# Optimization experiments

Measured on AMD Instinct MI355X. Metric: run time of the kernel, lower is better.

The kernel has to match this reference:

```python
import jax, jax.numpy as jnp
import numpy as np

B, N, D, DFC, EMB, L = 16, 1024, 128, 128, 64, 4
NHOPS = (1, 2, 3, 4)  # tatic='cont': nhop(i) = i + 1
EDGE_P = 0.03


def _make_adj(k):
    u = jax.random.uniform(k, (B, N, N))
    a = u < EDGE_P
    a = a | jnp.transpose(a, (0, 2, 1))          # undirected
    a = a | jnp.eye(N, dtype=bool)[None]         # self loops
    return a.astype(jnp.float32)


def setup_inputs() -> dict:
    key = jax.random.key(0)
    ks = jax.random.split(key, 16)
    s = 0.05
    x = jax.random.normal(ks[0], (B, N, 2 * EMB), jnp.float32)
    adj1 = _make_adj(ks[1])
    adj2 = _make_adj(ks[2])
    valid = jnp.ones((B, N), jnp.float32)
    embede_w = jax.random.normal(ks[3], (D, 2 * EMB)) * s
    gW = jax.random.normal(ks[4], (L, D, D)) * s
    gb = jnp.zeros((L, D), jnp.float32)
    gA = jax.random.normal(ks[5], (L, D, D)) * s
    gate_w = jax.random.normal(ks[6], (L, 1, 2 * D)) * s
    gate_b = jnp.zeros((L, 1), jnp.float32)
    fc0_w = jax.random.normal(ks[7], (DFC, D)) * s
    fc0_b = jnp.zeros((DFC,), jnp.float32)
    fc1_w = jax.random.normal(ks[8], (DFC, DFC)) * s
    fc1_b = jnp.zeros((DFC,), jnp.float32)
    fc2_w = jax.random.normal(ks[9], (DFC, DFC)) * s
    fc2_b = jnp.zeros((DFC,), jnp.float32)
    fc3_w = jax.random.normal(ks[10], (1, DFC)) * s
    fc3_b = jnp.zeros((1,), jnp.float32)
    return dict(x=x, adj1=adj1, adj2=adj2, valid=valid, embede_w=embede_w,
                gW=gW, gb=gb, gA=gA, gate_w=gate_w, gate_b=gate_b,
                fc0_w=fc0_w, fc0_b=fc0_b, fc1_w=fc1_w, fc1_b=fc1_b,
                fc2_w=fc2_w, fc2_b=fc2_b, fc3_w=fc3_w, fc3_b=fc3_b)


def _glema(x, adj, W, b, A, gw, gbias, nhop):
    h = x @ W.T + b                                        # [B,N,D]
    e = jnp.einsum('bjl,bkl->bjk', jnp.einsum('bjd,de->bje', h, A), h)
    e = e + jnp.transpose(e, (0, 2, 1))                    # undirected
    att = jnp.where(adj > 0, e, jnp.float32(0.0))
    att = jax.nn.softmax(att, axis=1) * adj                # softmax over dim 1, then adj mask
    az = jax.nn.relu(jnp.einsum('bij,bjd->bid', att, h))
    coeff = jax.nn.sigmoid(jnp.concatenate([h, az], -1) @ gw.T + gbias)  # [B,N,1]
    z = h
    for _ in range(nhop):
        az = jax.nn.relu(jnp.einsum('bij,bjd->bid', att, z))
        z = coeff * h + (1.0 - coeff) * az
    return z


def reference(x, adj1, adj2, valid, embede_w, gW, gb, gA, gate_w, gate_b,
              fc0_w, fc0_b, fc1_w, fc1_b, fc2_w, fc2_b, fc3_w, fc3_b):
    h = x @ embede_w.T                                     # embede (no bias)
    for k in range(L):                                     # branch='both': c_hs2 - c_hs1
        h1 = _glema(h, adj1, gW[k], gb[k], gA[k], gate_w[k], gate_b[k], NHOPS[k])
        h2 = _glema(h, adj2, gW[k], gb[k], gA[k], gate_w[k], gate_b[k], NHOPS[k])
        h = h2 - h1                                        # dropout p used in eval mode -> identity
    h = h * valid[..., None]
    pooled = h.sum(1) / valid.sum(1, keepdims=True)        # [B,D]
    y = jax.nn.relu(pooled @ fc0_w.T + fc0_b)
    y = jax.nn.relu(y @ fc1_w.T + fc1_b)
    y = jax.nn.relu(y @ fc2_w.T + fc2_b)
    y = jax.nn.sigmoid(y @ fc3_w.T + fc3_b)
    return y.reshape(-1)                                   # [B]
```

## Files before the change

### kernel.cpp

```cpp
#include <hip/hip_runtime.h>

typedef _Float16 half_t;
typedef _Float16 half8 __attribute__((ext_vector_type(8)));
typedef _Float16 half4v __attribute__((ext_vector_type(4)));
typedef float floatx4 __attribute__((ext_vector_type(4)));

#define MFMA(a,b,c) __builtin_amdgcn_mfma_f32_16x16x32_f16(a,b,c,0,0,0)

#define NB 16
#define NLEN 1024
#define DD 128
#define BN (NB*NLEN)
#define BND ((size_t)NB*NLEN*DD)
#define BNN ((size_t)NB*NLEN*NLEN)
#define ELLS 128
#define EMP 1044

static __device__ inline half_t f16h(unsigned pk) {
    unsigned short us = (unsigned short)(pk & 0xffffu);
    half_t h; __builtin_memcpy(&h, &us, 2); return h;
}

__global__ __launch_bounds__(256)
void k_pre(const float* __restrict__ adj1, const float* __restrict__ adj2,
           unsigned* __restrict__ ell, unsigned* __restrict__ cntA,
           const float* __restrict__ x, const float* __restrict__ Ew, half_t* __restrict__ h16,
           const float* __restrict__ gW, const float* __restrict__ gA,
           half_t* __restrict__ Wf, half_t* __restrict__ STf) {
    int tid = threadIdx.x;
    int bid = blockIdx.x;
    if (bid < 8192) {
        __shared__ unsigned ebuf[4][ELLS];
        int w = tid >> 6, l = tid & 63;
        int R = bid * 4 + w;
        int br = R >> 14, nb = R & 16383;
        const float* arow = (br ? adj2 : adj1) + (size_t)nb * 1024;
        unsigned* myb = ebuf[w];
        myb[l] = 0u; myb[l + 64] = 0u;
        float4 v0 = *(const float4*)&arow[l * 4];
        float4 v1 = *(const float4*)&arow[256 + l * 4];
        float4 v2 = *(const float4*)&arow[512 + l * 4];
        float4 v3 = *(const float4*)&arow[768 + l * 4];
        unsigned long long lmask = (l == 0) ? 0ull : (~0ull >> (64 - l));
        int base = 0;
        float vals[16] = {v0.x, v0.y, v0.z, v0.w, v1.x, v1.y, v1.z, v1.w,
                          v2.x, v2.y, v2.z, v2.w, v3.x, v3.y, v3.z, v3.w};
#pragma unroll
        for (int ch = 0; ch < 4; ch++) {
#pragma unroll
            for (int comp = 0; comp < 4; comp++) {
                bool pred = vals[ch * 4 + comp] > 0.f;
                unsigned long long b = __ballot(pred);
                if (pred) {
                    int idx = base + __popcll(b & lmask);
                    if (idx < ELLS) myb[idx] = ((unsigned)(ch * 256 + l * 4 + comp)) << 16;
                }
                base += __popcll(b);
            }
        }
        if (base > ELLS) base = ELLS;
        if (l == 0) cntA[R] = (unsigned)base;
        uint2 o = {myb[l * 2], myb[l * 2 + 1]};
        *(uint2*)&ell[(size_t)R * ELLS + l * 2] = o;
        return;
    }
    if (bid >= 10240) {
        int i = (bid - 10240) * 256 + tid;
        Wf[i] = (half_t)gW[i];
        int base = i & ~16383;
        int lrem = i & 16383;
        int d = lrem >> 7, e = lrem & 127;
        STf[base + (e << 7) + d] = (half_t)(gA[i] + gA[base + (e << 7) + d]);
        return;
    }
    __shared__ float rows[8][DD];
    int g = (bid - 8192) * 8;
    {
        int nl = tid >> 5, c4 = (tid & 31) * 4;
        *(float4*)&rows[nl][c4] = *(const float4*)&x[(size_t)(g + nl) * DD + c4];
    }
    __syncthreads();
    int t = tid & 127, half = tid >> 7;
    const float* wr = Ew + (size_t)t * DD;
    float acc[4] = {0.f, 0.f, 0.f, 0.f};
    for (int k = 0; k < DD; k++) {
        float w = wr[k];
#pragma unroll
        for (int m = 0; m < 4; m++) acc[m] += rows[half + 2 * m][k] * w;
    }
#pragma unroll
    for (int m = 0; m < 4; m++) h16[(size_t)(g + half + 2 * m) * DD + t] = (half_t)acc[m];
}

__global__ __launch_bounds__(256)
void k_proj(const half_t* __restrict__ pa, const half_t* __restrict__ pb,
            const half_t* __restrict__ Wf, const float* __restrict__ bias,
            const half_t* __restrict__ STf,
            half_t* __restrict__ hbr16, half_t* __restrict__ hbrF, half_t* __restrict__ hSF) {
    __shared__ half_t htile[32 * 136];
    __shared__ half_t hbtile[32 * 136];
    int g = blockIdx.x * 32;
    int t = threadIdx.x;
    int w = t >> 6, l = t & 63, q = l >> 4, l15 = l & 15;
#pragma unroll
    for (int v = 0; v < 2; v++) {
        int idx = v * 256 + t; int r = idx >> 4, c8 = (idx & 15) * 8;
        half8 va = *(const half8*)&pa[((size_t)(g + r) << 7) + c8];
        if (pb) {
            half8 vb = *(const half8*)&pb[((size_t)(g + r) << 7) + c8];
            va = va - vb;
        }
        *(half8*)&htile[r * 136 + c8] = va;
    }
    __syncthreads();
    int rowh = (w & 1) * 16;
    int c0 = (w >> 1) * 4;
    half8 a1[4];
#pragma unroll
    for (int kc = 0; kc < 4; kc++) a1[kc] = *(const half8*)&htile[(rowh + l15) * 136 + kc * 32 + q * 8];
    floatx4 acc[4];
#pragma unroll
    for (int cc = 0; cc < 4; cc++) {
        int col = (c0 + cc) * 16 + l15;
        floatx4 a = {0.f, 0.f, 0.f, 0.f};
#pragma unroll
        for (int kc = 0; kc < 4; kc++) {
            half8 bf = *(const half8*)&Wf[((size_t)col << 7) + kc * 32 + q * 8];
            a = MFMA(a1[kc], bf, a);
        }
        float bv = bias[col];
        a.x += bv; a.y += bv; a.z += bv; a.w += bv;
        acc[cc] = a;
    }
#pragma unroll
    for (int cc = 0; cc < 4; cc++) {
        int col = (c0 + cc) * 16 + l15;
#pragma unroll
        for (int r = 0; r < 4; r++)
            hbtile[(rowh + q * 4 + r) * 136 + col] = (half_t)acc[cc][r];
    }
    __syncthreads();
    half8 a2[4];
#pragma unroll
    for (int kc = 0; kc < 4; kc++) a2[kc] = *(const half8*)&hbtile[(rowh + l15) * 136 + kc * 32 + q * 8];
#pragma unroll
    for (int cc = 0; cc < 4; cc++) {
        int col = (c0 + cc) * 16 + l15;
        floatx4 a = {0.f, 0.f, 0.f, 0.f};
#pragma unroll
        for (int kc = 0; kc < 4; kc++) {
            half8 bf = *(const half8*)&STf[((size_t)col << 7) + kc * 32 + q * 8];
            a = MFMA(a2[kc], bf, a);
        }
        acc[cc] = a;
    }
    __syncthreads();
#pragma unroll
    for (int cc = 0; cc < 4; cc++) {
        int col = (c0 + cc) * 16 + l15;
#pragma unroll
        for (int r = 0; r < 4; r++) htile[(rowh + q * 4 + r) * 136 + col] = (half_t)acc[cc][r];
    }
    __syncthreads();
#pragma unroll
    for (int v = 0; v < 2; v++) {
        int idx = v * 256 + t; int r = idx >> 4, c8 = (idx & 15) * 8;
        *(half8*)&hbr16[((size_t)(g + r) << 7) + c8] = *(const half8*)&hbtile[r * 136 + c8];
    }
#pragma unroll
    for (int v = 0; v < 2; v++) {
        int fi = v * 256 + t;
        int g2 = fi >> 8, kc = (fi >> 6) & 3, li = fi & 63;
        int src = (g2 * 16 + (li & 15)) * 136 + kc * 32 + (li >> 4) * 8;
        size_t dst = (((size_t)(blockIdx.x * 2 + g2) * 4 + kc) << 10) + li * 8;
        *(half8*)&hbrF[dst] = *(const half8*)&hbtile[src];
        *(half8*)&hSF[dst]  = *(const half8*)&htile[src];
    }
}

__global__ __launch_bounds__(256)
void k_E(const half_t* __restrict__ hSF, const half_t* __restrict__ hbrF,
         const half_t* __restrict__ hbr16,
         unsigned* __restrict__ ell, const unsigned* __restrict__ cntA,
         float* __restrict__ rsr, half_t* __restrict__ hbrs) {
    int b = blockIdx.y, s = blockIdx.x;
    int t = threadIdx.x, w = t >> 6, l = t & 63, q = l >> 4, l15 = l & 15;
    __shared__ half_t emS[16 * EMP];
    __shared__ float rsS[2][16];
    size_t Gb = (size_t)b * 64;
    half8 A[4];
#pragma unroll
    for (int kc = 0; kc < 4; kc++)
        A[kc] = *(const half8*)&hSF[(((Gb + s) * 4 + kc) << 10) + l * 8];
#pragma unroll 4
    for (int cg = 0; cg < 16; cg++) {
        int c0 = w * 256 + cg * 16;
        floatx4 a = {0.f, 0.f, 0.f, 0.f};
#pragma unroll
        for (int kc = 0; kc < 4; kc++) {
            half8 bf = *(const half8*)&hbrF[(((Gb + w * 16 + cg) * 4 + kc) << 10) + l * 8];
            a = MFMA(A[kc], bf, a);
        }
#pragma unroll
        for (int r = 0; r < 4; r++)
            emS[(q * 4 + r) * EMP + c0 + l15] = (half_t)a[r];
    }
    __syncthreads();
    const float CN = 0.000335462627903f;
#pragma unroll
    for (int rr = 0; rr < 4; rr++) {
        int rl = w * 4 + rr;
        int rowg = b * 1024 + s * 16 + rl;
#pragma unroll
        for (int br = 0; br < 2; br++) {
            size_t R = ((size_t)br << 14) + rowg;
            int cn = (int)cntA[R];
            float rs = 0.f;
            for (int base = 0; base < cn; base += 64) {
                int si = base + l;
                float v = 0.f;
                if (si < cn) {
                    unsigned pk = ell[R * ELLS + si];
                    int col = (int)(pk >> 16);
                    float em = (float)emS[rl * EMP + col];
                    v = __expf(em - 8.f);
                    half_t hv = (half_t)v;
                    unsigned short us; __builtin_memcpy(&us, &hv, 2);
                    ((unsigned short*)ell)[(R * ELLS + si) * 2] = us;
                }
                rs += v;
            }
            rs += __shfl_xor(rs, 1); rs += __shfl_xor(rs, 2);
            rs += __shfl_xor(rs, 4); rs += __shfl_xor(rs, 8);
            rs += __shfl_xor(rs, 16); rs += __shfl_xor(rs, 32);
            if (l == 0) {
                float rv = 1.f / (rs + (1024.f - (float)cn) * CN);
                rsr[R] = rv;
                rsS[br][rl] = rv;
            }
        }
    }
    __syncthreads();
    const half_t* hrow = hbr16 + ((size_t)b << 17) + ((size_t)(s * 16) << 7);
#pragma unroll
    for (int v = 0; v < 2; v++) {
        int idx = v * 256 + t;
        int row = idx >> 5, br2 = (idx >> 4) & 1, ch = idx & 15;
        half8 hv = *(const half8*)&hrow[(size_t)row * 128 + ch * 8];
        float sc = rsS[br2][row];
        half8 o;
#pragma unroll
        for (int d = 0; d < 8; d++) o[d] = (half_t)(sc * (float)hv[d]);
        *(half8*)&hbrs[(size_t)br2 * BND + ((size_t)(b * 1024 + s * 16 + row) << 7) + ch * 8] = o;
    }
}

__global__ __launch_bounds__(256)
void k_az(const unsigned* __restrict__ ell, const unsigned* __restrict__ cntA,
          const float* __restrict__ rsr,
          const half_t* __restrict__ zin, const half_t* __restrict__ hbr16,
          const float* __restrict__ gw, const float* __restrict__ gb_,
          float* __restrict__ cfb, half_t* __restrict__ outp, int mode) {
    int t = threadIdx.x, w = t >> 6, l = t & 63;
    int g = l >> 4, l15 = l & 15;
    int R = blockIdx.x * 16 + w * 4 + g;
    int br = R >> 14, nb = R & 16383;
    const unsigned* ep = ell + (size_t)R * ELLS;
    int cn = (int)cntA[R];
    const half_t* zb = zin + (size_t)br * BND + (((size_t)(nb & ~1023)) << 7) + l15 * 8;
    half8 acc8 = {};
    uint4 p4 = *(const uint4*)ep;
    for (int s = 0; s < cn; s += 4) {
        uint4 cur = p4;
        p4 = *(const uint4*)(ep + s + 4);
        unsigned pk[4] = {cur.x, cur.y, cur.z, cur.w};
#pragma unroll
        for (int i = 0; i < 4; i++) {
            half8 zz = *(const half8*)(zb + (((size_t)(pk[i] >> 16)) << 7));
            half_t hv = f16h(pk[i]);
            half8 vv = {hv, hv, hv, hv, hv, hv, hv, hv};
            acc8 += zz * vv;
        }
    }
    float acc[8];
#pragma unroll
    for (int d = 0; d < 8; d++) acc[d] = fmaxf((float)acc8[d], 0.f);
    half8 hv8 = *(const half8*)&hbr16[((size_t)nb << 7) + l15 * 8];
    float hv[8];
#pragma unroll
    for (int d = 0; d < 8; d++) hv[d] = (float)hv8[d];
    float cf;
    if (mode >= 3) {
        const float* g1 = gw + l15 * 8;
        const float* g2 = gw + 128 + l15 * 8;
        float dp = 0.f;
#pragma unroll
        for (int d = 0; d < 8; d++) dp += hv[d] * g1[d] + acc[d] * g2[d];
        dp += __shfl_xor(dp, 1); dp += __shfl_xor(dp, 2);
        dp += __shfl_xor(dp, 4); dp += __shfl_xor(dp, 8);
        cf = 1.f / (1.f + __expf(-(dp + gb_[0])));
        if (l15 == 0) cfb[R] = cf;
    } else {
        cf = cfb[R];
    }
    float sc = (mode == 1 || mode == 3) ? rsr[R] : 1.f;
    half8 o;
#pragma unroll
    for (int d = 0; d < 8; d++)
        o[d] = (half_t)(sc * (cf * hv[d] + (1.f - cf) * acc[d]));
    *(half8*)&outp[(size_t)R * DD + l15 * 8] = o;
}

__global__ __launch_bounds__(256)
void k_pool(const half_t* __restrict__ z2, const half_t* __restrict__ z1,
            const float* __restrict__ valid, float* __restrict__ part) {
    int b = blockIdx.y, s = blockIdx.x;
    int t = threadIdx.x, d = t & 127, hf = t >> 7;
    __shared__ float red[128];
    float acc = 0.f;
    int nbase = s * 128 + hf * 64;
    for (int n = nbase; n < nbase + 64; n++) {
        size_t gi = ((size_t)(b * 1024 + n) << 7) + d;
        acc += ((float)z2[gi] - (float)z1[gi]) * valid[b * 1024 + n];
    }
    if (hf) red[d] = acc;
    __syncthreads();
    if (!hf) part[(b * 8 + s) * 128 + d] = acc + red[d];
}

__global__ __launch_bounds__(128)
void k_mlp(const float* __restrict__ part, const float* __restrict__ valid,
           const float* __restrict__ w0, const float* __restrict__ b0,
           const float* __restrict__ w1, const float* __restrict__ b1,
           const float* __restrict__ w2, const float* __restrict__ b2,
           const float* __restrict__ w3, const float* __restrict__ b3,
           float* __restrict__ out) {
    int b = blockIdx.x, t = threadIdx.x;
    __shared__ float y0[DD], y1[DD];
    __shared__ float sred[2];
    float vs = 0.f;
    for (int n = t; n < NLEN; n += 128) vs += valid[b * NLEN + n];
    for (int off = 32; off; off >>= 1) vs += __shfl_down(vs, off);
    if ((t & 63) == 0) sred[t >> 6] = vs;
    __syncthreads();
    float vsum = sred[0] + sred[1];
    float acc = 0.f;
#pragma unroll
    for (int s = 0; s < 8; s++) acc += part[(b * 8 + s) * 128 + t];
    y0[t] = acc / vsum;
    __syncthreads();
    float a = b0[t];
    for (int k = 0; k < DD; k++) a += y0[k] * w0[t * DD + k];
    y1[t] = fmaxf(a, 0.f);
    __syncthreads();
    a = b1[t];
    for (int k = 0; k < DD; k++) a += y1[k] * w1[t * DD + k];
    y0[t] = fmaxf(a, 0.f);
    __syncthreads();
    a = b2[t];
    for (int k = 0; k < DD; k++) a += y0[k] * w2[t * DD + k];
    y1[t] = fmaxf(a, 0.f);
    __syncthreads();
    float p = y1[t] * w3[t];
    for (int off = 32; off; off >>= 1) p += __shfl_down(p, off);
    if ((t & 63) == 0) sred[t >> 6] = p;
    __syncthreads();
    if (t == 0) out[b] = 1.f / (1.f + __expf(-(sred[0] + sred[1] + b3[0])));
}

extern "C" void kernel_launch(void* const* d_in, const int* in_sizes, int n_in,
                              void* d_out, int out_size, void* d_ws, size_t ws_size,
                              hipStream_t stream) {
    (void)in_sizes; (void)n_in; (void)out_size; (void)ws_size;
    const float* x     = (const float*)d_in[0];
    const float* adj1  = (const float*)d_in[1];
    const float* adj2  = (const float*)d_in[2];
    const float* valid = (const float*)d_in[3];
    const float* Ew    = (const float*)d_in[4];
    const float* gW    = (const float*)d_in[5];
    const float* gb    = (const float*)d_in[6];
    const float* gA    = (const float*)d_in[7];
    const float* gatew = (const float*)d_in[8];
    const float* gateb = (const float*)d_in[9];
    const float* w0 = (const float*)d_in[10]; const float* b0 = (const float*)d_in[11];
    const float* w1 = (const float*)d_in[12]; const float* b1 = (const float*)d_in[13];
    const float* w2 = (const float*)d_in[14]; const float* b2 = (const float*)d_in[15];
    const float* w3 = (const float*)d_in[16]; const float* b3 = (const float*)d_in[17];
    float* out = (float*)d_out;

    char* p = (char*)d_ws;
    float* rsr  = (float*)p; p += 2 * BN * 4;
    float* cfb  = (float*)p; p += 2 * BN * 4;
    float* partb = (float*)p; p += (size_t)NB * 8 * 128 * 4;
    half_t* h16   = (half_t*)p; p += BND * 2;
    half_t* hbr16 = (half_t*)p; p += BND * 2;
    half_t* hbrF  = (half_t*)p; p += BND * 2;
    half_t* hSF   = (half_t*)p; p += BND * 2;
    half_t* hbrs  = (half_t*)p; p += 2 * BND * 2;
    half_t* zf    = (half_t*)p; p += 2 * BND * 2;
    half_t* zsA   = (half_t*)p; p += 2 * BND * 2;
    half_t* zsB   = (half_t*)p; p += 2 * BND * 2;
    unsigned* ell = (unsigned*)p; p += (size_t)2 * BN * ELLS * 4 + 16;
    unsigned* cntA = (unsigned*)p; p += (size_t)2 * BN * 4;
    half_t* Wf16 = (half_t*)p; p += (size_t)4 * 128 * 128 * 2;
    half_t* ST16 = (half_t*)p; p += (size_t)4 * 128 * 128 * 2;

    k_pre<<<10496, 256, 0, stream>>>(adj1, adj2, ell, cntA, x, Ew, h16, gW, gA, Wf16, ST16);

    for (int k = 0; k < 4; k++) {
        int nhop = k + 1;
        const half_t* pa = k ? (zf + BND) : h16;
        const half_t* pb = k ? zf : nullptr;
        k_proj<<<512, 256, 0, stream>>>(pa, pb, Wf16 + (size_t)k * 16384, gb + k * 128,
                                        ST16 + (size_t)k * 16384, hbr16, hbrF, hSF);
        k_E<<<dim3(64, NB), 256, 0, stream>>>(hSF, hbrF, hbr16, ell, cntA, rsr, hbrs);
        half_t* tgate = (nhop == 1) ? zf : zsA;
        k_az<<<2048, 256, 0, stream>>>(ell, cntA, rsr, hbrs, hbr16,
                                       gatew + k * 256, gateb + k, cfb, tgate,
                                       (nhop == 1) ? 4 : 3);
        half_t* src = tgate;
        for (int hop = 2; hop <= nhop; hop++) {
            half_t* dst = (hop == nhop) ? zf : ((hop & 1) ? zsA : zsB);
            k_az<<<2048, 256, 0, stream>>>(ell, cntA, rsr, src, hbr16,
                                           gatew + k * 256, gateb + k, cfb, dst,
                                           (hop == nhop) ? 2 : 1);
            src = dst;
        }
    }
    k_pool<<<dim3(8, NB), 256, 0, stream>>>(zf + BND, zf, valid, partb);
    k_mlp<<<16, 128, 0, stream>>>(partb, valid, w0, b0, w1, b1, w2, b2, w3, b3, out);
}
```

Measured before the change: 697.4 us.

## Fuse all stages into one persistent cooperative kernel with grid syncs

Replaces the chain of roughly two dozen kernel launches (preprocess, per-layer projection, attention/E, hop aggregation, pooling, MLP) with a single cooperative kernel. Each stage becomes a grid-stride loop over its former blocks, separated by grid-wide barriers, and all stages share one shared-memory union. The aim is to remove launch gaps and the idle tail between dependent kernels. In exchange, the whole kernel must fit the largest stage's shared memory and register footprint, which can lower occupancy for the light aggregation stages, and each grid barrier has its own cost. The original multi-launch path is kept as a fallback if the cooperative launch fails.

```diff
diff --git a/kernel.cpp b/kernel.cpp
--- a/kernel.cpp
+++ b/kernel.cpp
@@ -1,8 +1,9 @@
 #include <hip/hip_runtime.h>
+#include <hip/hip_cooperative_groups.h>
+namespace cg = cooperative_groups;
 
 typedef _Float16 half_t;
 typedef _Float16 half8 __attribute__((ext_vector_type(8)));
-typedef _Float16 half4v __attribute__((ext_vector_type(4)));
 typedef float floatx4 __attribute__((ext_vector_type(4)));
 
 #define MFMA(a,b,c) __builtin_amdgcn_mfma_f32_16x16x32_f16(a,b,c,0,0,0)
@@ -12,7 +13,6 @@
 #define DD 128
 #define BN (NB*NLEN)
 #define BND ((size_t)NB*NLEN*DD)
-#define BNN ((size_t)NB*NLEN*NLEN)
 #define ELLS 128
 #define EMP 1044
 
@@ -21,60 +21,57 @@
     half_t h; __builtin_memcpy(&h, &us, 2); return h;
 }
 
-__global__ __launch_bounds__(256)
-void k_pre(const float* __restrict__ adj1, const float* __restrict__ adj2,
+union SMem {
+    struct { unsigned ebuf[4][ELLS]; } pre;
+    struct { float rows[8][DD]; } emb;
+    struct { half_t htile[32 * 136]; half_t hbtile[32 * 136]; } proj;
+    struct { half_t emS[16 * EMP]; float rsS[2][16]; } E;
+    struct { float red[128]; } pool;
+    struct { float y0[DD]; float y1[DD]; float sred[2]; } mlp;
+};
+
+__device__ __forceinline__
+void d_ell(int wid, const float* __restrict__ adj1, const float* __restrict__ adj2,
            unsigned* __restrict__ ell, unsigned* __restrict__ cntA,
-           const float* __restrict__ x, const float* __restrict__ Ew, half_t* __restrict__ h16,
-           const float* __restrict__ gW, const float* __restrict__ gA,
-           half_t* __restrict__ Wf, half_t* __restrict__ STf) {
+           unsigned (*ebuf)[ELLS]) {
+    int tid = threadIdx.x, w = tid >> 6, l = tid & 63;
+    int R = wid * 4 + w;
+    int br = R >> 14, nb = R & 16383;
+    const float* arow = (br ? adj2 : adj1) + (size_t)nb * 1024;
+    unsigned* myb = ebuf[w];
+    myb[l] = 0u; myb[l + 64] = 0u;
+    float4 v0 = *(const float4*)&arow[l * 4];
+    float4 v1 = *(const float4*)&arow[256 + l * 4];
+    float4 v2 = *(const float4*)&arow[512 + l * 4];
+    float4 v3 = *(const float4*)&arow[768 + l * 4];
+    unsigned long long lmask = (l == 0) ? 0ull : (~0ull >> (64 - l));
+    int base = 0;
+    float vals[16] = {v0.x, v0.y, v0.z, v0.w, v1.x, v1.y, v1.z, v1.w,
+                      v2.x, v2.y, v2.z, v2.w, v3.x, v3.y, v3.z, v3.w};
+#pragma unroll
+    for (int ch = 0; ch < 4; ch++) {
+#pragma unroll
+        for (int comp = 0; comp < 4; comp++) {
+            bool pred = vals[ch * 4 + comp] > 0.f;
+            unsigned long long b = __ballot(pred);
+            if (pred) {
+                int idx = base + __popcll(b & lmask);
+                if (idx < ELLS) myb[idx] = ((unsigned)(ch * 256 + l * 4 + comp)) << 16;
+            }
+            base += __popcll(b);
+        }
+    }
+    if (base > ELLS) base = ELLS;
+    if (l == 0) cntA[R] = (unsigned)base;
+    uint2 o = {myb[l * 2], myb[l * 2 + 1]};
+    *(uint2*)&ell[(size_t)R * ELLS + l * 2] = o;
+}
+
+__device__ __forceinline__
+void d_embed(int wid, const float* __restrict__ x, const float* __restrict__ Ew,
+             half_t* __restrict__ h16, float (*rows)[DD]) {
     int tid = threadIdx.x;
-    int bid = blockIdx.x;
-    if (bid < 8192) {
-        __shared__ unsigned ebuf[4][ELLS];
-        int w = tid >> 6, l = tid & 63;
-        int R = bid * 4 + w;
-        int br = R >> 14, nb = R & 16383;
-        const float* arow = (br ? adj2 : adj1) + (size_t)nb * 1024;
-        unsigned* myb = ebuf[w];
-        myb[l] = 0u; myb[l + 64] = 0u;
-        float4 v0 = *(const float4*)&arow[l * 4];
-        float4 v1 = *(const float4*)&arow[256 + l * 4];
-        float4 v2 = *(const float4*)&arow[512 + l * 4];
-        float4 v3 = *(const float4*)&arow[768 + l * 4];
-        unsigned long long lmask = (l == 0) ? 0ull : (~0ull >> (64 - l));
-        int base = 0;
-        float vals[16] = {v0.x, v0.y, v0.z, v0.w, v1.x, v1.y, v1.z, v1.w,
-                          v2.x, v2.y, v2.z, v2.w, v3.x, v3.y, v3.z, v3.w};
-#pragma unroll
-        for (int ch = 0; ch < 4; ch++) {
-#pragma unroll
-            for (int comp = 0; comp < 4; comp++) {
-                bool pred = vals[ch * 4 + comp] > 0.f;
-                unsigned long long b = __ballot(pred);
-                if (pred) {
-                    int idx = base + __popcll(b & lmask);
-                    if (idx < ELLS) myb[idx] = ((unsigned)(ch * 256 + l * 4 + comp)) << 16;
-                }
-                base += __popcll(b);
-            }
-        }
-        if (base > ELLS) base = ELLS;
-        if (l == 0) cntA[R] = (unsigned)base;
-        uint2 o = {myb[l * 2], myb[l * 2 + 1]};
-        *(uint2*)&ell[(size_t)R * ELLS + l * 2] = o;
-        return;
-    }
-    if (bid >= 10240) {
-        int i = (bid - 10240) * 256 + tid;
-        Wf[i] = (half_t)gW[i];
-        int base = i & ~16383;
-        int lrem = i & 16383;
-        int d = lrem >> 7, e = lrem & 127;
-        STf[base + (e << 7) + d] = (half_t)(gA[i] + gA[base + (e << 7) + d]);
-        return;
-    }
-    __shared__ float rows[8][DD];
-    int g = (bid - 8192) * 8;
+    int g = wid * 8;
     {
         int nl = tid >> 5, c4 = (tid & 31) * 4;
         *(float4*)&rows[nl][c4] = *(const float4*)&x[(size_t)(g + nl) * DD + c4];
@@ -92,14 +89,24 @@
     for (int m = 0; m < 4; m++) h16[(size_t)(g + half + 2 * m) * DD + t] = (half_t)acc[m];
 }
 
-__global__ __launch_bounds__(256)
-void k_proj(const half_t* __restrict__ pa, const half_t* __restrict__ pb,
+__device__ __forceinline__
+void d_wcast(int wid, const float* __restrict__ gW, const float* __restrict__ gA,
+             half_t* __restrict__ Wf, half_t* __restrict__ STf) {
+    int i = wid * 256 + threadIdx.x;
+    Wf[i] = (half_t)gW[i];
+    int base = i & ~16383;
+    int lrem = i & 16383;
+    int d = lrem >> 7, e = lrem & 127;
+    STf[base + (e << 7) + d] = (half_t)(gA[i] + gA[base + (e << 7) + d]);
+}
+
+__device__ __forceinline__
+void d_proj(int wid, const half_t* __restrict__ pa, const half_t* __restrict__ pb,
             const half_t* __restrict__ Wf, const float* __restrict__ bias,
             const half_t* __restrict__ STf,
-            half_t* __restrict__ hbr16, half_t* __restrict__ hbrF, half_t* __restrict__ hSF) {
-    __shared__ half_t htile[32 * 136];
-    __shared__ half_t hbtile[32 * 136];
-    int g = blockIdx.x * 32;
+            half_t* __restrict__ hbr16, half_t* __restrict__ hbrF, half_t* __restrict__ hSF,
+            half_t* __restrict__ htile, half_t* __restrict__ hbtile) {
+    int g = wid * 32;
     int t = threadIdx.x;
     int w = t >> 6, l = t & 63, q = l >> 4, l15 = l & 15;
 #pragma unroll
@@ -172,33 +179,32 @@
         int fi = v * 256 + t;
         int g2 = fi >> 8, kc = (fi >> 6) & 3, li = fi & 63;
         int src = (g2 * 16 + (li & 15)) * 136 + kc * 32 + (li >> 4) * 8;
-        size_t dst = (((size_t)(blockIdx.x * 2 + g2) * 4 + kc) << 10) + li * 8;
+        size_t dst = (((size_t)(wid * 2 + g2) * 4 + kc) << 10) + li * 8;
         *(half8*)&hbrF[dst] = *(const half8*)&hbtile[src];
         *(half8*)&hSF[dst]  = *(const half8*)&htile[src];
     }
 }
 
-__global__ __launch_bounds__(256)
-void k_E(const half_t* __restrict__ hSF, const half_t* __restrict__ hbrF,
+__device__ __forceinline__
+void d_E(int wid, const half_t* __restrict__ hSF, const half_t* __restrict__ hbrF,
          const half_t* __restrict__ hbr16,
          unsigned* __restrict__ ell, const unsigned* __restrict__ cntA,
-         float* __restrict__ rsr, half_t* __restrict__ hbrs) {
-    int b = blockIdx.y, s = blockIdx.x;
+         float* __restrict__ rsr, half_t* __restrict__ hbrs,
+         half_t* __restrict__ emS, float (*rsS)[16]) {
+    int b = wid >> 6, s = wid & 63;
     int t = threadIdx.x, w = t >> 6, l = t & 63, q = l >> 4, l15 = l & 15;
-    __shared__ half_t emS[16 * EMP];
-    __shared__ float rsS[2][16];
     size_t Gb = (size_t)b * 64;
     half8 A[4];
 #pragma unroll
     for (int kc = 0; kc < 4; kc++)
         A[kc] = *(const half8*)&hSF[(((Gb + s) * 4 + kc) << 10) + l * 8];
 #pragma unroll 4
-    for (int cg = 0; cg < 16; cg++) {
-        int c0 = w * 256 + cg * 16;
+    for (int cg2 = 0; cg2 < 16; cg2++) {
+        int c0 = w * 256 + cg2 * 16;
         floatx4 a = {0.f, 0.f, 0.f, 0.f};
 #pragma unroll
         for (int kc = 0; kc < 4; kc++) {
-            half8 bf = *(const half8*)&hbrF[(((Gb + w * 16 + cg) * 4 + kc) << 10) + l * 8];
+            half8 bf = *(const half8*)&hbrF[(((Gb + w * 16 + cg2) * 4 + kc) << 10) + l * 8];
             a = MFMA(A[kc], bf, a);
         }
 #pragma unroll
@@ -255,15 +261,15 @@
     }
 }
 
-__global__ __launch_bounds__(256)
-void k_az(const unsigned* __restrict__ ell, const unsigned* __restrict__ cntA,
+__device__ __forceinline__
+void d_az(int wid, const unsigned* __restrict__ ell, const unsigned* __restrict__ cntA,
           const float* __restrict__ rsr,
           const half_t* __restrict__ zin, const half_t* __restrict__ hbr16,
           const float* __restrict__ gw, const float* __restrict__ gb_,
           float* __restrict__ cfb, half_t* __restrict__ outp, int mode) {
     int t = threadIdx.x, w = t >> 6, l = t & 63;
     int g = l >> 4, l15 = l & 15;
-    int R = blockIdx.x * 16 + w * 4 + g;
+    int R = wid * 16 + w * 4 + g;
     int br = R >> 14, nb = R & 16383;
     const unsigned* ep = ell + (size_t)R * ELLS;
     int cn = (int)cntA[R];
@@ -311,12 +317,12 @@
     *(half8*)&outp[(size_t)R * DD + l15 * 8] = o;
 }
 
-__global__ __launch_bounds__(256)
-void k_pool(const half_t* __restrict__ z2, const half_t* __restrict__ z1,
-            const float* __restrict__ valid, float* __restrict__ part) {
-    int b = blockIdx.y, s = blockIdx.x;
+__device__ __forceinline__
+void d_pool(int wid, const half_t* __restrict__ z2, const half_t* __restrict__ z1,
+            const float* __restrict__ valid, float* __restrict__ part,
+            float* __restrict__ red) {
+    int b = wid >> 3, s = wid & 7;
     int t = threadIdx.x, d = t & 127, hf = t >> 7;
-    __shared__ float red[128];
     float acc = 0.f;
     int nbase = s * 128 + hf * 64;
     for (int n = nbase; n < nbase + 64; n++) {
@@ -328,16 +334,14 @@
     if (!hf) part[(b * 8 + s) * 128 + d] = acc + red[d];
 }
 
-__global__ __launch_bounds__(128)
-void k_mlp(const float* __restrict__ part, const float* __restrict__ valid,
+__device__ __forceinline__
+void d_mlp(int b, int t, const float* __restrict__ part, const float* __restrict__ valid,
            const float* __restrict__ w0, const float* __restrict__ b0,
            const float* __restrict__ w1, const float* __restrict__ b1,
            const float* __restrict__ w2, const float* __restrict__ b2,
            const float* __restrict__ w3, const float* __restrict__ b3,
-           float* __restrict__ out) {
-    int b = blockIdx.x, t = threadIdx.x;
-    __shared__ float y0[DD], y1[DD];
-    __shared__ float sred[2];
+           float* __restrict__ out, float* __restrict__ y0, float* __restrict__ y1,
+           float* __restrict__ sred) {
     float vs = 0.f;
     for (int n = t; n < NLEN; n += 128) vs += valid[b * NLEN + n];
     for (int off = 32; off; off >>= 1) vs += __shfl_down(vs, off);
@@ -368,65 +372,202 @@
     if (t == 0) out[b] = 1.f / (1.f + __expf(-(sred[0] + sred[1] + b3[0])));
 }
 
+struct KParams {
+    const float *adj1, *adj2, *x, *Ew, *gW, *gA, *gb, *gatew, *gateb;
+    const float *valid, *w0, *b0, *w1, *b1, *w2, *b2, *w3, *b3;
+    float *rsr, *cfb, *partb, *out;
+    half_t *h16, *hbr16, *hbrF, *hSF, *hbrs, *zf, *zsA, *zsB, *Wf, *STf;
+    unsigned *ell, *cntA;
+};
+
+__global__ __launch_bounds__(256)
+void k_all(KParams P) {
+    cg::grid_group gg = cg::this_grid();
+    __shared__ SMem sm;
+    int G = gridDim.x;
+    for (int wid = blockIdx.x; wid < 10496; wid += G) {
+        if (wid < 8192) {
+            d_ell(wid, P.adj1, P.adj2, P.ell, P.cntA, sm.pre.ebuf);
+        } else if (wid >= 10240) {
+            d_wcast(wid - 10240, P.gW, P.gA, P.Wf, P.STf);
+        } else {
+            d_embed(wid - 8192, P.x, P.Ew, P.h16, sm.emb.rows);
+            __syncthreads();
+        }
+    }
+    gg.sync();
+    for (int k = 0; k < 4; k++) {
+        int nhop = k + 1;
+        const half_t* pa = k ? (P.zf + BND) : P.h16;
+        const half_t* pb = k ? P.zf : nullptr;
+        const half_t* Wfk = P.Wf + (size_t)k * 16384;
+        const half_t* STk = P.STf + (size_t)k * 16384;
+        const float* biask = P.gb + k * 128;
+        const float* gwk = P.gatew + k * 256;
+        const float* gbk = P.gateb + k;
+        for (int wid = blockIdx.x; wid < 512; wid += G) {
+            d_proj(wid, pa, pb, Wfk, biask, STk, P.hbr16, P.hbrF, P.hSF,
+                   sm.proj.htile, sm.proj.hbtile);
+            __syncthreads();
+        }
+        gg.sync();
+        for (int wid = blockIdx.x; wid < 1024; wid += G) {
+            d_E(wid, P.hSF, P.hbrF, P.hbr16, P.ell, P.cntA, P.rsr, P.hbrs,
+                sm.E.emS, sm.E.rsS);
+            __syncthreads();
+        }
+        gg.sync();
+        half_t* tgate = (nhop == 1) ? P.zf : P.zsA;
+        for (int wid = blockIdx.x; wid < 2048; wid += G)
+            d_az(wid, P.ell, P.cntA, P.rsr, P.hbrs, P.hbr16, gwk, gbk, P.cfb,
+                 tgate, (nhop == 1) ? 4 : 3);
+        gg.sync();
+        half_t* src = tgate;
+        for (int hop = 2; hop <= nhop; hop++) {
+            half_t* dst = (hop == nhop) ? P.zf : ((hop & 1) ? P.zsA : P.zsB);
+            for (int wid = blockIdx.x; wid < 2048; wid += G)
+                d_az(wid, P.ell, P.cntA, P.rsr, src, P.hbr16, gwk, gbk, P.cfb,
+                     dst, (hop == nhop) ? 2 : 1);
+            gg.sync();
+            src = dst;
+        }
+    }
+    for (int wid = blockIdx.x; wid < 128; wid += G) {
+        d_pool(wid, P.zf + BND, P.zf, P.valid, P.partb, sm.pool.red);
+        __syncthreads();
+    }
+    gg.sync();
+    for (int wid = blockIdx.x; wid < 16; wid += G) {
+        d_mlp(wid, threadIdx.x & 127, P.partb, P.valid, P.w0, P.b0, P.w1, P.b1,
+              P.w2, P.b2, P.w3, P.b3, P.out, sm.mlp.y0, sm.mlp.y1, sm.mlp.sred);
+        __syncthreads();
+    }
+}
+
+__global__ __launch_bounds__(256)
+void k_pre(const float* adj1, const float* adj2, unsigned* ell, unsigned* cntA,
+           const float* x, const float* Ew, half_t* h16,
+           const float* gW, const float* gA, half_t* Wf, half_t* STf) {
+    __shared__ SMem sm;
+    int bid = blockIdx.x;
+    if (bid < 8192) d_ell(bid, adj1, adj2, ell, cntA, sm.pre.ebuf);
+    else if (bid >= 10240) d_wcast(bid - 10240, gW, gA, Wf, STf);
+    else d_embed(bid - 8192, x, Ew, h16, sm.emb.rows);
+}
+
+__global__ __launch_bounds__(256)
+void k_proj(const half_t* pa, const half_t* pb, const half_t* Wf, const float* bias,
+            const half_t* STf, half_t* hbr16, half_t* hbrF, half_t* hSF) {
+    __shared__ SMem sm;
+    d_proj(blockIdx.x, pa, pb, Wf, bias, STf, hbr16, hbrF, hSF,
+           sm.proj.htile, sm.proj.hbtile);
+}
+
+__global__ __launch_bounds__(256)
+void k_E(const half_t* hSF, const half_t* hbrF, const half_t* hbr16,
+         unsigned* ell, const unsigned* cntA, float* rsr, half_t* hbrs) {
+    __shared__ SMem sm;
+    d_E(blockIdx.y * 64 + blockIdx.x, hSF, hbrF, hbr16, ell, cntA, rsr, hbrs,
+        sm.E.emS, sm.E.rsS);
+}
+
+__global__ __launch_bounds__(256)
+void k_az(const unsigned* ell, const unsigned* cntA, const float* rsr,
+          const half_t* zin, const half_t* hbr16, const float* gw, const float* gb_,
+          float* cfb, half_t* outp, int mode) {
+    d_az(blockIdx.x, ell, cntA, rsr, zin, hbr16, gw, gb_, cfb, outp, mode);
+}
+
+__global__ __launch_bounds__(256)
+void k_pool(const half_t* z2, const half_t* z1, const float* valid, float* part) {
+    __shared__ SMem sm;
+    d_pool(blockIdx.y * 8 + blockIdx.x, z2, z1, valid, part, sm.pool.red);
+}
+
+__global__ __launch_bounds__(128)
+void k_mlp(const float* part, const float* valid,
+           const float* w0, const float* b0, const float* w1, const float* b1,
+           const float* w2, const float* b2, const float* w3, const float* b3,
+           float* out) {
+    __shared__ float y0[DD], y1[DD], sred[2];
+    d_mlp(blockIdx.x, threadIdx.x, part, valid, w0, b0, w1, b1, w2, b2, w3, b3,
+          out, y0, y1, sred);
+}
+
 extern "C" void kernel_launch(void* const* d_in, const int* in_sizes, int n_in,
                               void* d_out, int out_size, void* d_ws, size_t ws_size,
                               hipStream_t stream) {
     (void)in_sizes; (void)n_in; (void)out_size; (void)ws_size;
-    const float* x     = (const float*)d_in[0];
-    const float* adj1  = (const float*)d_in[1];
-    const float* adj2  = (const float*)d_in[2];
-    const float* valid = (const float*)d_in[3];
-    const float* Ew    = (const float*)d_in[4];
-    const float* gW    = (const float*)d_in[5];
-    const float* gb    = (const float*)d_in[6];
-    const float* gA    = (const float*)d_in[7];
-    const float* gatew = (const float*)d_in[8];
-    const float* gateb = (const float*)d_in[9];
-    const float* w0 = (const float*)d_in[10]; const float* b0 = (const float*)d_in[11];
-    const float* w1 = (const float*)d_in[12]; const float* b1 = (const float*)d_in[13];
-    const float* w2 = (const float*)d_in[14]; const float* b2 = (const float*)d_in[15];
-    const float* w3 = (const float*)d_in[16]; const float* b3 = (const float*)d_in[17];
-    float* out = (float*)d_out;
+    KParams P;
+    P.x     = (const float*)d_in[0];
+    P.adj1  = (const float*)d_in[1];
+    P.adj2  = (const float*)d_in[2];
+    P.valid = (const float*)d_in[3];
+    P.Ew    = (const float*)d_in[4];
+    P.gW    = (const float*)d_in[5];
+    P.gb    = (const float*)d_in[6];
+    P.gA    = (const float*)d_in[7];
+    P.gatew = (const float*)d_in[8];
+    P.gateb = (const float*)d_in[9];
+    P.w0 = (const float*)d_in[10]; P.b0 = (const float*)d_in[11];
+    P.w1 = (const float*)d_in[12]; P.b1 = (const float*)d_in[13];
+    P.w2 = (const float*)d_in[14]; P.b2 = (const float*)d_in[15];
+    P.w3 = (const float*)d_in[16]; P.b3 = (const float*)d_in[17];
+    P.out = (float*)d_out;
 
     char* p = (char*)d_ws;
-    float* rsr  = (float*)p; p += 2 * BN * 4;
-    float* cfb  = (float*)p; p += 2 * BN * 4;
-    float* partb = (float*)p; p += (size_t)NB * 8 * 128 * 4;
-    half_t* h16   = (half_t*)p; p += BND * 2;
-    half_t* hbr16 = (half_t*)p; p += BND * 2;
-    half_t* hbrF  = (half_t*)p; p += BND * 2;
-    half_t* hSF   = (half_t*)p; p += BND * 2;
-    half_t* hbrs  = (half_t*)p; p += 2 * BND * 2;
-    half_t* zf    = (half_t*)p; p += 2 * BND * 2;
-    half_t* zsA   = (half_t*)p; p += 2 * BND * 2;
-    half_t* zsB   = (half_t*)p; p += 2 * BND * 2;
-    unsigned* ell = (unsigned*)p; p += (size_t)2 * BN * ELLS * 4 + 16;
-    unsigned* cntA = (unsigned*)p; p += (size_t)2 * BN * 4;
-    half_t* Wf16 = (half_t*)p; p += (size_t)4 * 128 * 128 * 2;
-    half_t* ST16 = (half_t*)p; p += (size_t)4 * 128 * 128 * 2;
-
-    k_pre<<<10496, 256, 0, stream>>>(adj1, adj2, ell, cntA, x, Ew, h16, gW, gA, Wf16, ST16);
-
+    P.rsr  = (float*)p; p += 2 * BN * 4;
+    P.cfb  = (float*)p; p += 2 * BN * 4;
+    P.partb = (float*)p; p += (size_t)NB * 8 * 128 * 4;
+    P.h16   = (half_t*)p; p += BND * 2;
+    P.hbr16 = (half_t*)p; p += BND * 2;
+    P.hbrF  = (half_t*)p; p += BND * 2;
+    P.hSF   = (half_t*)p; p += BND * 2;
+    P.hbrs  = (half_t*)p; p += 2 * BND * 2;
+    P.zf    = (half_t*)p; p += 2 * BND * 2;
+    P.zsA   = (half_t*)p; p += 2 * BND * 2;
+    P.zsB   = (half_t*)p; p += 2 * BND * 2;
+    P.ell = (unsigned*)p; p += (size_t)2 * BN * ELLS * 4 + 16;
+    P.cntA = (unsigned*)p; p += (size_t)2 * BN * 4;
+    P.Wf = (half_t*)p; p += (size_t)4 * 128 * 128 * 2;
+    P.STf = (half_t*)p; p += (size_t)4 * 128 * 128 * 2;
+
+    int occ = 0;
+    hipError_t oe = hipOccupancyMaxActiveBlocksPerMultiprocessor(
+        &occ, reinterpret_cast<const void*>(&k_all), 256, 0);
+    if (oe != hipSuccess || occ < 1) occ = 2;
+    int grid = occ * 256;
+    if (grid > 2048) grid = 2048;
+
+    void* args[] = { (void*)&P };
+    hipError_t e = hipLaunchCooperativeKernel(reinterpret_cast<const void*>(&k_all),
+                                              dim3(grid), dim3(256), args, 0, stream);
+    if (e == hipSuccess) return;
+
+    k_pre<<<10496, 256, 0, stream>>>(P.adj1, P.adj2, P.ell, P.cntA, P.x, P.Ew, P.h16,
+                                     P.gW, P.gA, P.Wf, P.STf);
     for (int k = 0; k < 4; k++) {
         int nhop = k + 1;
-        const half_t* pa = k ? (zf + BND) : h16;
-        const half_t* pb = k ? zf : nullptr;
-        k_proj<<<512, 256, 0, stream>>>(pa, pb, Wf16 + (size_t)k * 16384, gb + k * 128,
-                                        ST16 + (size_t)k * 16384, hbr16, hbrF, hSF);
-        k_E<<<dim3(64, NB), 256, 0, stream>>>(hSF, hbrF, hbr16, ell, cntA, rsr, hbrs);
-        half_t* tgate = (nhop == 1) ? zf : zsA;
-        k_az<<<2048, 256, 0, stream>>>(ell, cntA, rsr, hbrs, hbr16,
-                                       gatew + k * 256, gateb + k, cfb, tgate,
+        const half_t* pa = k ? (P.zf + BND) : P.h16;
+        const half_t* pb = k ? P.zf : nullptr;
+        k_proj<<<512, 256, 0, stream>>>(pa, pb, P.Wf + (size_t)k * 16384, P.gb + k * 128,
+                                        P.STf + (size_t)k * 16384, P.hbr16, P.hbrF, P.hSF);
+        k_E<<<dim3(64, NB), 256, 0, stream>>>(P.hSF, P.hbrF, P.hbr16, P.ell, P.cntA,
+                                              P.rsr, P.hbrs);
+        half_t* tgate = (nhop == 1) ? P.zf : P.zsA;
+        k_az<<<2048, 256, 0, stream>>>(P.ell, P.cntA, P.rsr, P.hbrs, P.hbr16,
+                                       P.gatew + k * 256, P.gateb + k, P.cfb, tgate,
                                        (nhop == 1) ? 4 : 3);
         half_t* src = tgate;
         for (int hop = 2; hop <= nhop; hop++) {
-            half_t* dst = (hop == nhop) ? zf : ((hop & 1) ? zsA : zsB);
-            k_az<<<2048, 256, 0, stream>>>(ell, cntA, rsr, src, hbr16,
-                                           gatew + k * 256, gateb + k, cfb, dst,
+            half_t* dst = (hop == nhop) ? P.zf : ((hop & 1) ? P.zsA : P.zsB);
+            k_az<<<2048, 256, 0, stream>>>(P.ell, P.cntA, P.rsr, src, P.hbr16,
+                                           P.gatew + k * 256, P.gateb + k, P.cfb, dst,
                                            (hop == nhop) ? 2 : 1);
             src = dst;
         }
     }
-    k_pool<<<dim3(8, NB), 256, 0, stream>>>(zf + BND, zf, valid, partb);
-    k_mlp<<<16, 128, 0, stream>>>(partb, valid, w0, b0, w1, b1, w2, b2, w3, b3, out);
-}
+    k_pool<<<dim3(8, NB), 256, 0, stream>>>(P.zf + BND, P.zf, P.valid, P.partb);
+    k_mlp<<<16, 128, 0, stream>>>(P.partb, P.valid, P.w0, P.b0, P.w1, P.b1,
+                                  P.w2, P.b2, P.w3, P.b3, P.out);
+}
```

Measured after the change: 1.939 ms. 2.78x slower.
